# Kernel tuning notes

Measured on AMD Instinct MI355X. Metric: run time of the kernel, lower is better.

Reference implementation:

```python
import jax, jax.numpy as jnp
import numpy as np

# NF4 codebook (bitsandbytes quant_type='nf4'), 16 fixed quantile values
NF4 = jnp.array([
    -1.0, -0.6961928009986877, -0.5250730514526367, -0.39491748809814453,
    -0.28444138169288635, -0.18477343022823334, -0.09105003625154495, 0.0,
    0.07958029955625534, 0.16093020141124725, 0.24611230194568634,
    0.33791524171829224, 0.44070982933044434, 0.5626170039176941,
    0.7229568362236023, 1.0], dtype=jnp.float32)
BLK = 64  # bnb default blocksize for nf4


def dequant_nf4(codes, absmax):
    # codes: [out, in] int codes in [0,16); absmax: [out, in//BLK] blockwise scale
    out_f, in_f = codes.shape
    w = NF4[codes].reshape(out_f, in_f // BLK, BLK) * absmax[:, :, None]
    return w.reshape(out_f, in_f)


def setup_inputs() -> dict:
    key = jax.random.key(0)
    ks = jax.random.split(key, 7)
    hd, m, T = 4096, 14336, 2048
    x = jax.random.normal(ks[0], (T, hd), dtype=jnp.float32)
    gate_codes = jax.random.randint(ks[1], (m, hd), 0, 16, dtype=jnp.int32)
    gate_absmax = jax.random.uniform(ks[2], (m, hd // BLK), dtype=jnp.float32) * 0.05
    up_codes = jax.random.randint(ks[3], (m, hd), 0, 16, dtype=jnp.int32)
    up_absmax = jax.random.uniform(ks[4], (m, hd // BLK), dtype=jnp.float32) * 0.05
    down_codes = jax.random.randint(ks[5], (hd, m), 0, 16, dtype=jnp.int32)
    down_absmax = jax.random.uniform(ks[6], (hd, m // BLK), dtype=jnp.float32) * 0.05
    return {"x": x, "gate_codes": gate_codes, "gate_absmax": gate_absmax,
            "up_codes": up_codes, "up_absmax": up_absmax,
            "down_codes": down_codes, "down_absmax": down_absmax}


def reference(x, gate_codes, gate_absmax, up_codes, up_absmax, down_codes, down_absmax):
    # SwiGLU MLP: down( silu(gate(x)) * up(x) ), weights dequantized from nf4
    Wg = dequant_nf4(gate_codes, gate_absmax)   # [m, hd]
    Wu = dequant_nf4(up_codes, up_absmax)       # [m, hd]
    Wd = dequant_nf4(down_codes, down_absmax)   # [hd, m]
    g = x @ Wg.T                                # [T, m]
    h = jax.nn.silu(g) * (x @ Wu.T)             # [T, m]
    return h @ Wd.T                             # [T, hd]
```

## Files before the change

kernel.cpp:

```cpp
#include <hip/hip_runtime.h>
#include <hip/hip_bf16.h>
#include <cstdint>
#include <cstddef>

#define TDIM 2048
#define HDIM 4096
#define MDIM 14336

typedef __attribute__((ext_vector_type(8))) __bf16 bf16x8;
typedef __attribute__((ext_vector_type(4))) float f32x4;

__device__ __constant__ float NF4_LUT[16] = {
    -1.0f, -0.6961928009986877f, -0.5250730514526367f, -0.39491748809814453f,
    -0.28444138169288635f, -0.18477343022823334f, -0.09105003625154495f, 0.0f,
    0.07958029955625534f, 0.16093020141124725f, 0.24611230194568634f,
    0.33791524171829224f, 0.44070982933044434f, 0.5626170039176941f,
    0.7229568362236023f, 1.0f};

__device__ __forceinline__ void g2l16(const void* g, void* l) {
  __builtin_amdgcn_global_load_lds(
      (const __attribute__((address_space(1))) unsigned int*)g,
      (__attribute__((address_space(3))) unsigned int*)l, 16, 0, 0);
}

__global__ __launch_bounds__(256) void f32_to_bf16_k(
    const float* __restrict__ in, __hip_bfloat16* __restrict__ out, int n8) {
  for (int i = blockIdx.x * 256 + threadIdx.x; i < n8; i += gridDim.x * 256) {
    const float4* p = (const float4*)(in + (size_t)i * 8);
    float4 a = p[0], b = p[1];
    union { __hip_bfloat16 h[8]; int4 v; } u;
    u.h[0] = __float2bfloat16(a.x);
    u.h[1] = __float2bfloat16(a.y);
    u.h[2] = __float2bfloat16(a.z);
    u.h[3] = __float2bfloat16(a.w);
    u.h[4] = __float2bfloat16(b.x);
    u.h[5] = __float2bfloat16(b.y);
    u.h[6] = __float2bfloat16(b.z);
    u.h[7] = __float2bfloat16(b.w);
    *(int4*)(out + (size_t)i * 8) = u.v;
  }
}

__global__ __launch_bounds__(256) void dequant_nf4_k(
    const int* __restrict__ codes, const float* __restrict__ absmax,
    __hip_bfloat16* __restrict__ W, int K) {
  __shared__ float lut[16];
  if (threadIdx.x < 16) lut[threadIdx.x] = NF4_LUT[threadIdx.x];
  __syncthreads();
  const int row = blockIdx.x;
  const int K8 = K >> 3;
  const size_t rbase = (size_t)row * K;
  for (int c8 = threadIdx.x; c8 < K8; c8 += 256) {
    const int col = c8 << 3;
    const float am = absmax[(size_t)row * (K >> 6) + (col >> 6)];
    const int4* cp = (const int4*)(codes + rbase + col);
    int4 ca = cp[0], cb = cp[1];
    union { __hip_bfloat16 h[8]; int4 v; } u;
    u.h[0] = __float2bfloat16(lut[ca.x & 15] * am);
    u.h[1] = __float2bfloat16(lut[ca.y & 15] * am);
    u.h[2] = __float2bfloat16(lut[ca.z & 15] * am);
    u.h[3] = __float2bfloat16(lut[ca.w & 15] * am);
    u.h[4] = __float2bfloat16(lut[cb.x & 15] * am);
    u.h[5] = __float2bfloat16(lut[cb.y & 15] * am);
    u.h[6] = __float2bfloat16(lut[cb.z & 15] * am);
    u.h[7] = __float2bfloat16(lut[cb.w & 15] * am);
    *(int4*)(W + rbase + col) = u.v;
  }
}

template <int EPI>
__global__ __launch_bounds__(256, 4) void gemm_nt_k(
    const __hip_bfloat16* __restrict__ A, const __hip_bfloat16* __restrict__ B,
    void* __restrict__ Cv, const __hip_bfloat16* __restrict__ Gin,
    int M, int N, int Kfull, int Kloc, int ksplit) {
  __shared__ __align__(16) char sA[128 * 128];
  __shared__ __align__(16) char sB[128 * 128];

  const int tid = threadIdx.x;
  const int lane = tid & 63;
  const int wid = tid >> 6;
  const int wm = wid >> 1, wn = wid & 1;

  const int nbn = N >> 7;
  const int nwg2 = (M >> 7) * nbn;
  const int G = nwg2 * ksplit;
  const int q8 = G >> 3;
  const int bid = blockIdx.x;
  const int wg = (bid & 7) * q8 + (bid >> 3);
  const int kh = wg / nwg2;
  const int rem = wg - kh * nwg2;
  const int bm = rem / nbn;
  const int bn = rem - bm * nbn;

  const size_t Kb = (size_t)Kfull * 2;
  const size_t koffb = (size_t)kh * Kloc * 2;

  const int srow = lane >> 3;
  const int scw = ((lane & 7) ^ srow) << 4;
  const uint8_t* gA = (const uint8_t*)A +
      (size_t)(bm * 128 + wid * 8 + srow) * Kb + koffb + scw;
  const uint8_t* gB = (const uint8_t*)B +
      (size_t)(bn * 128 + wid * 8 + srow) * Kb + koffb + scw;
  char* lA = sA + wid * 1024;
  char* lB = sB + wid * 1024;

  const int colsw = (((lane >> 4) << 4) ^ ((lane & 7) << 4));
  const char* aRd = sA + (wm * 64 + (lane & 15)) * 128 + colsw;
  const char* bRd = sB + (wn * 64 + (lane & 15)) * 128 + colsw;

  f32x4 acc[4][4] = {};

  const int nt = Kloc >> 6;
  for (int kt = 0; kt < nt; ++kt) {
    const size_t kb = (size_t)kt * 128;
#pragma unroll
    for (int s = 0; s < 4; ++s) {
      g2l16(gA + (size_t)(s * 32) * Kb + kb, lA + s * 4096);
      g2l16(gB + (size_t)(s * 32) * Kb + kb, lB + s * 4096);
    }
    __syncthreads();
#pragma unroll
    for (int ks = 0; ks < 2; ++ks) {
      bf16x8 af[4], bv[4];
#pragma unroll
      for (int i = 0; i < 4; ++i) {
        af[i] = *(const bf16x8*)((uintptr_t)(aRd + i * 2048) ^ (ks << 6));
        bv[i] = *(const bf16x8*)((uintptr_t)(bRd + i * 2048) ^ (ks << 6));
      }
#pragma unroll
      for (int mi = 0; mi < 4; ++mi)
#pragma unroll
        for (int nj = 0; nj < 4; ++nj)
          acc[mi][nj] = __builtin_amdgcn_mfma_f32_16x16x32_bf16(
              af[mi], bv[nj], acc[mi][nj], 0, 0, 0);
    }
    __syncthreads();
  }

  const int row0 = bm * 128 + wm * 64 + ((lane >> 4) << 2);
  const int col0 = bn * 128 + wn * 64 + (lane & 15);
#pragma unroll
  for (int mi = 0; mi < 4; ++mi) {
#pragma unroll
    for (int nj = 0; nj < 4; ++nj) {
#pragma unroll
      for (int r = 0; r < 4; ++r) {
        const size_t idx =
            (size_t)(row0 + mi * 16 + r) * N + (col0 + nj * 16);
        const float v = acc[mi][nj][r];
        if (EPI == 0) {
          ((__hip_bfloat16*)Cv)[idx] = __float2bfloat16(v);
        } else if (EPI == 1) {
          const float g = __bfloat162float(Gin[idx]);
          ((__hip_bfloat16*)Cv)[idx] =
              __float2bfloat16(g / (1.0f + __expf(-g)) * v);
        } else {
          atomicAdd(&((float*)Cv)[idx], v);
        }
      }
    }
  }
}

extern "C" void kernel_launch(void* const* d_in, const int* in_sizes, int n_in,
                              void* d_out, int out_size, void* d_ws,
                              size_t ws_size, hipStream_t stream) {
  const float* x = (const float*)d_in[0];
  const int* gate_codes = (const int*)d_in[1];
  const float* gate_absmax = (const float*)d_in[2];
  const int* up_codes = (const int*)d_in[3];
  const float* up_absmax = (const float*)d_in[4];
  const int* down_codes = (const int*)d_in[5];
  const float* down_absmax = (const float*)d_in[6];

  char* ws = (char*)d_ws;
  __hip_bfloat16* xb = (__hip_bfloat16*)ws;
  __hip_bfloat16* Wb = (__hip_bfloat16*)(ws + (size_t)TDIM * HDIM * 2);
  __hip_bfloat16* Hb = (__hip_bfloat16*)(ws + (size_t)TDIM * HDIM * 2 +
                                         (size_t)MDIM * HDIM * 2);

  hipMemsetAsync(d_out, 0, (size_t)TDIM * HDIM * 4, stream);

  f32_to_bf16_k<<<2048, 256, 0, stream>>>(x, xb, (TDIM * HDIM) / 8);

  dequant_nf4_k<<<MDIM, 256, 0, stream>>>(gate_codes, gate_absmax, Wb, HDIM);
  gemm_nt_k<0><<<(TDIM / 128) * (MDIM / 128), 256, 0, stream>>>(
      xb, Wb, Hb, nullptr, TDIM, MDIM, HDIM, HDIM, 1);
  dequant_nf4_k<<<MDIM, 256, 0, stream>>>(up_codes, up_absmax, Wb, HDIM);
  gemm_nt_k<1><<<(TDIM / 128) * (MDIM / 128), 256, 0, stream>>>(
      xb, Wb, Hb, Hb, TDIM, MDIM, HDIM, HDIM, 1);
  dequant_nf4_k<<<HDIM, 256, 0, stream>>>(down_codes, down_absmax, Wb, MDIM);
  gemm_nt_k<2><<<2 * (TDIM / 128) * (HDIM / 128), 256, 0, stream>>>(
      Hb, Wb, (float*)d_out, nullptr, TDIM, HDIM, MDIM, MDIM / 2, 2);
}
```

Measured before the change: 1.133 ms.

## Double-buffer LDS tiles in GEMM and reorder block mapping column-major

Doubles the shared-memory A/B buffers so the global-to-LDS loads for the next K tile are issued before computing on the current one. Explicit vmcnt waits and raw barriers replace __syncthreads so one stage of loads stays in flight, hiding global memory latency behind MFMA work. It also swaps the tile index decomposition so consecutive workgroups walk along M instead of N, which changes L2 reuse. LDS per block doubles to 64KB and launch bounds drop to 2 blocks per CU, reducing occupancy.

```diff
diff --git a/kernel.cpp b/kernel.cpp
--- a/kernel.cpp
+++ b/kernel.cpp
@@ -69,28 +69,29 @@
 }
 
 template <int EPI>
-__global__ __launch_bounds__(256, 4) void gemm_nt_k(
+__global__ __launch_bounds__(256, 2) void gemm_nt_k(
     const __hip_bfloat16* __restrict__ A, const __hip_bfloat16* __restrict__ B,
     void* __restrict__ Cv, const __hip_bfloat16* __restrict__ Gin,
     int M, int N, int Kfull, int Kloc, int ksplit) {
-  __shared__ __align__(16) char sA[128 * 128];
-  __shared__ __align__(16) char sB[128 * 128];
+  __shared__ __align__(16) char sA[2 * 128 * 128];
+  __shared__ __align__(16) char sB[2 * 128 * 128];
 
   const int tid = threadIdx.x;
   const int lane = tid & 63;
   const int wid = tid >> 6;
   const int wm = wid >> 1, wn = wid & 1;
 
+  const int nbm = M >> 7;
   const int nbn = N >> 7;
-  const int nwg2 = (M >> 7) * nbn;
+  const int nwg2 = nbm * nbn;
   const int G = nwg2 * ksplit;
   const int q8 = G >> 3;
   const int bid = blockIdx.x;
   const int wg = (bid & 7) * q8 + (bid >> 3);
   const int kh = wg / nwg2;
   const int rem = wg - kh * nwg2;
-  const int bm = rem / nbn;
-  const int bn = rem - bm * nbn;
+  const int bn = rem / nbm;
+  const int bm = rem - bn * nbm;
 
   const size_t Kb = (size_t)Kfull * 2;
   const size_t koffb = (size_t)kh * Kloc * 2;
@@ -101,8 +102,17 @@
       (size_t)(bm * 128 + wid * 8 + srow) * Kb + koffb + scw;
   const uint8_t* gB = (const uint8_t*)B +
       (size_t)(bn * 128 + wid * 8 + srow) * Kb + koffb + scw;
-  char* lA = sA + wid * 1024;
-  char* lB = sB + wid * 1024;
+
+  auto stage = [&](int kt, int b) {
+    const size_t kb = (size_t)kt * 128;
+    char* la = sA + b * 16384 + wid * 1024;
+    char* lb = sB + b * 16384 + wid * 1024;
+#pragma unroll
+    for (int s = 0; s < 4; ++s) {
+      g2l16(gA + (size_t)(s * 32) * Kb + kb, la + s * 4096);
+      g2l16(gB + (size_t)(s * 32) * Kb + kb, lb + s * 4096);
+    }
+  };
 
   const int colsw = (((lane >> 4) << 4) ^ ((lane & 7) << 4));
   const char* aRd = sA + (wm * 64 + (lane & 15)) * 128 + colsw;
@@ -111,21 +121,26 @@
   f32x4 acc[4][4] = {};
 
   const int nt = Kloc >> 6;
+  stage(0, 0);
   for (int kt = 0; kt < nt; ++kt) {
-    const size_t kb = (size_t)kt * 128;
-#pragma unroll
-    for (int s = 0; s < 4; ++s) {
-      g2l16(gA + (size_t)(s * 32) * Kb + kb, lA + s * 4096);
-      g2l16(gB + (size_t)(s * 32) * Kb + kb, lB + s * 4096);
-    }
-    __syncthreads();
+    const int cur = kt & 1;
+    if (kt + 1 < nt) {
+      stage(kt + 1, cur ^ 1);
+      asm volatile("s_waitcnt vmcnt(8)" ::: "memory");
+    } else {
+      asm volatile("s_waitcnt vmcnt(0)" ::: "memory");
+    }
+    __builtin_amdgcn_s_barrier();
+    asm volatile("" ::: "memory");
+    const char* aR = aRd + cur * 16384;
+    const char* bR = bRd + cur * 16384;
 #pragma unroll
     for (int ks = 0; ks < 2; ++ks) {
       bf16x8 af[4], bv[4];
 #pragma unroll
       for (int i = 0; i < 4; ++i) {
-        af[i] = *(const bf16x8*)((uintptr_t)(aRd + i * 2048) ^ (ks << 6));
-        bv[i] = *(const bf16x8*)((uintptr_t)(bRd + i * 2048) ^ (ks << 6));
+        af[i] = *(const bf16x8*)((uintptr_t)(aR + i * 2048) ^ (ks << 6));
+        bv[i] = *(const bf16x8*)((uintptr_t)(bR + i * 2048) ^ (ks << 6));
       }
 #pragma unroll
       for (int mi = 0; mi < 4; ++mi)
@@ -134,7 +149,9 @@
           acc[mi][nj] = __builtin_amdgcn_mfma_f32_16x16x32_bf16(
               af[mi], bv[nj], acc[mi][nj], 0, 0, 0);
     }
-    __syncthreads();
+    asm volatile("" ::: "memory");
+    __builtin_amdgcn_s_barrier();
+    asm volatile("" ::: "memory");
   }
 
   const int row0 = bm * 128 + wm * 64 + ((lane >> 4) << 2);
```

Result: slower. 1.272 ms (+12.2%).
